# Performance work log

Measured on AMD Instinct MI355X. Metric: run time of the kernel, lower is better.

## Reference

```python
import jax, jax.numpy as jnp
import numpy as np

BN_EPS = 1e-5


def _gcn(x, A, W, gamma, beta):
    # x: [B,N,Cin], A: [B,N,N] -> [B,N,Cout]; BatchNorm1d over (B,N) per channel (train-mode batch stats)
    h = jnp.einsum('bnm,bmc->bnc', A, x @ W)
    mu = h.mean(axis=(0, 1))
    var = h.var(axis=(0, 1))
    h = (h - mu) * jax.lax.rsqrt(var + BN_EPS) * gamma + beta
    return jax.nn.relu(h)  # dropout is identity (drop_prob=0 / eval)


def _ppige(x, A, W0, g0, b0, W_res, g_res, b_res):
    h = _gcn(x, A, W0, g0, b0)
    for i in range(W_res.shape[0]):  # residual GCN stack (num_GCN-1 layers)
        h = _gcn(h, A, W_res[i], g_res[i], b_res[i]) + h
    return h


def _gge(x, w1, b1, w2, b2):
    return jax.nn.relu(jax.nn.relu(x @ w1 + b1) @ w2 + b2)


def _gaga(G, h):
    # G: [B,N,H], h: [B,H]
    att = jax.nn.softmax(jnp.einsum('bnh,bh->bn', G, h), axis=-1)
    return jnp.einsum('bnh,bn->bh', G, att)


def _led(ea, eb, conv_w, conv_b, p1_w, p1_b, p2_w, p2_b):
    # ea, eb: [B, 2H]; Conv1d(2H->2H, k=1) over length-2 axis then MaxPool1d(2)
    stacked = jnp.stack([ea, eb], axis=-1)  # [B, 2H, 2]
    conv = jnp.einsum('oc,bct->bot', conv_w, stacked) + conv_b[None, :, None]
    cnn_x = conv.max(axis=-1)  # [B, 2H]
    x = jax.nn.relu(jnp.concatenate([cnn_x, ea - eb], axis=1) @ p1_w + p1_b)
    return x @ p2_w + p2_b


def setup_inputs() -> dict:
    key = jax.random.key(0)
    ks = jax.random.split(key, 24)
    Bs, N, PPI_in, H, F_in = 8, 2048, 512, 256, 1024
    n_res = 3  # num_GCN - 1
    s = 0.02
    adjA = jax.random.uniform(ks[0], (Bs, N, N), jnp.float32)
    adjB = jax.random.uniform(ks[1], (Bs, N, N), jnp.float32)
    adjA = adjA / adjA.sum(-1, keepdims=True)  # row-normalized for numerical sanity
    adjB = adjB / adjB.sum(-1, keepdims=True)
    return {
        'a': jax.random.normal(ks[2], (Bs, F_in), jnp.float32),
        'bio_a': jax.random.normal(ks[3], (Bs, N, PPI_in), jnp.float32),
        'A': adjA,
        'b': jax.random.normal(ks[4], (Bs, F_in), jnp.float32),
        'bio_b': jax.random.normal(ks[5], (Bs, N, PPI_in), jnp.float32),
        'B': adjB,
        'W0': jax.random.normal(ks[6], (PPI_in, H), jnp.float32) * s,
        'gamma0': jnp.ones((H,), jnp.float32),
        'beta0': jnp.zeros((H,), jnp.float32),
        'W_res': jax.random.normal(ks[7], (n_res, H, H), jnp.float32) * s,
        'gamma_res': jnp.ones((n_res, H), jnp.float32),
        'beta_res': jnp.zeros((n_res, H), jnp.float32),
        'g1_w': jax.random.normal(ks[8], (F_in, 128), jnp.float32) * s,
        'g1_b': jnp.zeros((128,), jnp.float32),
        'g2_w': jax.random.normal(ks[9], (128, H), jnp.float32) * s,
        'g2_b': jnp.zeros((H,), jnp.float32),
        'conv_w': jax.random.normal(ks[10], (2 * H, 2 * H), jnp.float32) * s,
        'conv_b': jnp.zeros((2 * H,), jnp.float32),
        'p1_w': jax.random.normal(ks[11], (4 * H, H), jnp.float32) * s,
        'p1_b': jnp.zeros((H,), jnp.float32),
        'p2_w': jax.random.normal(ks[12], (H, 2), jnp.float32) * s,
        'p2_b': jnp.zeros((2,), jnp.float32),
    }


def reference(a, bio_a, A, b, bio_b, B, W0, gamma0, beta0, W_res, gamma_res, beta_res,
              g1_w, g1_b, g2_w, g2_b, conv_w, conv_b, p1_w, p1_b, p2_w, p2_b):
    Ga = _ppige(bio_a, A, W0, gamma0, beta0, W_res, gamma_res, beta_res)
    Gb = _ppige(bio_b, B, W0, gamma0, beta0, W_res, gamma_res, beta_res)
    ha = _gge(a, g1_w, g1_b, g2_w, g2_b)
    hb = _gge(b, g1_w, g1_b, g2_w, g2_b)
    ea = jnp.concatenate([ha, _gaga(Ga, ha)], axis=-1)
    eb = jnp.concatenate([hb, _gaga(Gb, hb)], axis=-1)
    logits = _led(ea, eb, conv_w, conv_b, p1_w, p1_b, p2_w, p2_b)
    return jax.nn.log_softmax(logits, axis=-1)
```

## Files before the change

kernel.cpp:

```cpp
#include <hip/hip_runtime.h>
#include <hip/hip_bf16.h>
#include <cstdint>

typedef unsigned short u16;
typedef __bf16 bf16x8 __attribute__((ext_vector_type(8)));
typedef float f32x4 __attribute__((ext_vector_type(4)));

typedef __attribute__((address_space(1))) const void* gas_ptr;
typedef __attribute__((address_space(3))) void* las_ptr;

__device__ __forceinline__ u16 f2bf(float f) {
  union { __hip_bfloat16 h; u16 u; } v;
  v.h = __float2bfloat16(f);
  return v.u;
}
__device__ __forceinline__ float bf2f(u16 u) {
  union { unsigned int i; float f; } v;
  v.i = ((unsigned int)u) << 16;
  return v.f;
}

__device__ __forceinline__ void gload16(const u16* g, u16* l) {
  __builtin_amdgcn_global_load_lds((gas_ptr)g, (las_ptr)l, 16, 0, 0);
}

__global__ __launch_bounds__(256) void k_prep_weights(const float* __restrict__ W0,
                                                      const float* __restrict__ Wres,
                                                      u16* __restrict__ W0t,
                                                      u16* __restrict__ Wrt) {
  __shared__ float tile[32][33];
  int y = blockIdx.y;
  const float* src; u16* dst; int R, r0;
  if (y < 16) { src = W0; dst = W0t; R = 512; r0 = y * 32; }
  else {
    int i = (y - 16) >> 3;
    src = Wres + i * 65536; dst = Wrt + i * 65536; R = 256; r0 = ((y - 16) & 7) * 32;
  }
  const int C = 256;
  int c0 = blockIdx.x * 32;
  int tx = threadIdx.x & 31, ty = threadIdx.x >> 5;
#pragma unroll
  for (int i = 0; i < 4; ++i) {
    int r = ty + i * 8;
    tile[r][tx] = src[(long)(r0 + r) * C + c0 + tx];
  }
  __syncthreads();
#pragma unroll
  for (int i = 0; i < 4; ++i) {
    int c = ty + i * 8;
    dst[(long)(c0 + c) * R + r0 + tx] = f2bf(tile[tx][c]);
  }
}

template<int EPI, int SWZ, int CVT>
__global__ __launch_bounds__(256, 3) void k_gemm(
    const u16* __restrict__ A, int lda, long sA,
    const float* __restrict__ Afa, const float* __restrict__ Afb,
    long splitRow, int ldaf, long zrows, u16* __restrict__ AbfOut,
    const u16* __restrict__ Bt, int ldb, long sB,
    u16* __restrict__ C, int ldc, long sC,
    u16* __restrict__ PtOut, int ldpt,
    float* __restrict__ stats, int K) {
  __shared__ __align__(16) u16 smem[24576];
  __shared__ float cs[256];
  const int tid = threadIdx.x;
  const int lane = tid & 63;
  const int wid = tid >> 6;
  const int wm = wid >> 1, wn = wid & 1;

  int bx = blockIdx.x, by = blockIdx.y, bz = blockIdx.z;
  if (SWZ == 1) {
    int lin = bx + 16 * by + 32 * bz;
    int swz = (lin & 7) * 64 + (lin >> 3);
    bx = swz & 15; by = (swz >> 4) & 1; bz = swz >> 5;
  } else if (SWZ == 2) {
    int t = bx; bx = by; by = t;
  }
  const long m0 = (long)bx * 128, n0 = (long)by * 128;
  const int z = bz;
  const u16* Ab = A + (long)z * sA;
  const u16* Btb = Bt + (long)z * sB;

  const int rsub = lane >> 3;
  const int swzcol = ((lane & 7) ^ rsub) * 8;
  const long a_row = m0 + wid * 32 + rsub;
  const long b_row = n0 + wid * 32 + rsub;

  if (EPI == 0) cs[tid] = 0.f;

  const f32x4 zero = {0.f, 0.f, 0.f, 0.f};
  f32x4 acc[4][4];
#pragma unroll
  for (int i = 0; i < 4; ++i)
#pragma unroll
    for (int j = 0; j < 4; ++j) acc[i][j] = zero;

  const int fr = lane & 15;
  const int kgrp = lane >> 4;
  const int swz_rd = lane & 7;
  const int nk = K >> 6;

  float4 rgf[8];
  uint4 rgu[4];

  auto stageB = [&](int bufofs, int k0) {
#pragma unroll
    for (int i = 0; i < 4; ++i)
      gload16(Btb + (b_row + i * 8) * (long)ldb + (k0 + swzcol),
              &smem[bufofs + (wid * 32 + i * 8) * 64]);
  };
  auto loadA = [&](int k0) {
    if constexpr (CVT) {
#pragma unroll
      for (int i = 0; i < 4; ++i) {
        long R = (long)z * zrows + a_row + i * 8;
        const float* sp = (R < splitRow ? Afa + R * (long)ldaf
                                        : Afb + (R - splitRow) * (long)ldaf) + k0 + swzcol;
        rgf[i * 2] = *reinterpret_cast<const float4*>(sp);
        rgf[i * 2 + 1] = *reinterpret_cast<const float4*>(sp + 4);
      }
    } else {
#pragma unroll
      for (int i = 0; i < 4; ++i)
        rgu[i] = *reinterpret_cast<const uint4*>(Ab + (a_row + i * 8) * (long)lda + k0 + swzcol);
    }
  };
  auto writeA = [&](int k0) {
#pragma unroll
    for (int i = 0; i < 4; ++i) {
      uint4 q;
      if constexpr (CVT) {
        union { u16 u[8]; uint4 qq; } o;
        o.u[0] = f2bf(rgf[i*2].x);   o.u[1] = f2bf(rgf[i*2].y);
        o.u[2] = f2bf(rgf[i*2].z);   o.u[3] = f2bf(rgf[i*2].w);
        o.u[4] = f2bf(rgf[i*2+1].x); o.u[5] = f2bf(rgf[i*2+1].y);
        o.u[6] = f2bf(rgf[i*2+1].z); o.u[7] = f2bf(rgf[i*2+1].w);
        q = o.qq;
        if (AbfOut && by == 0) {
          long R = (long)z * zrows + a_row + i * 8;
          *reinterpret_cast<uint4*>(AbfOut + R * (long)ldaf + k0 + swzcol) = q;
        }
      } else {
        q = rgu[i];
      }
      *reinterpret_cast<uint4*>(&smem[(wid * 32 + i * 8) * 64 + lane * 8]) = q;
    }
  };
  auto compute = [&](const u16* Asb, const u16* Bsb) {
#pragma unroll
    for (int ks = 0; ks < 2; ++ks) {
      bf16x8 af[4], bfv[4];
#pragma unroll
      for (int f = 0; f < 4; ++f) {
        int cA = (ks * 4 + kgrp) ^ swz_rd;
        af[f]  = *reinterpret_cast<const bf16x8*>(&Asb[(wm * 64 + f * 16 + fr) * 64 + cA * 8]);
        bfv[f] = *reinterpret_cast<const bf16x8*>(&Bsb[(wn * 64 + f * 16 + fr) * 64 + cA * 8]);
      }
#pragma unroll
      for (int mf = 0; mf < 4; ++mf)
#pragma unroll
        for (int nf = 0; nf < 4; ++nf)
          acc[mf][nf] = __builtin_amdgcn_mfma_f32_16x16x32_bf16(af[mf], bfv[nf], acc[mf][nf], 0, 0, 0);
    }
  };

  stageB(8192, 0);
  loadA(0);
  writeA(0);
  __syncthreads();
  for (int t = 0; t < nk; ++t) {
    const u16* Bsb = &smem[8192 + ((t & 1) << 13)];
    if (t + 1 < nk) {
      stageB(8192 + ((~t & 1) << 13), (t + 1) * 64);
      loadA((t + 1) * 64);
    }
    compute(smem, Bsb);
    __syncthreads();
    if (t + 1 < nk) writeA((t + 1) * 64);
    __syncthreads();
  }

  if (EPI == 0) {
    u16* Cb = C + (long)z * sC;
    const int side = z >> 3;
#pragma unroll
    for (int mf = 0; mf < 4; ++mf) {
      long mrow = m0 + wm * 64 + mf * 16 + kgrp * 4;
#pragma unroll
      for (int nf = 0; nf < 4; ++nf) {
        long ncol = n0 + wn * 64 + nf * 16 + fr;
#pragma unroll
        for (int r = 0; r < 4; ++r)
          Cb[(mrow + r) * ldc + ncol] = f2bf(acc[mf][nf][r]);
      }
    }
#pragma unroll
    for (int nf = 0; nf < 4; ++nf) {
      int cl = wn * 64 + nf * 16 + fr;
      float s = 0.f, q = 0.f;
#pragma unroll
      for (int mf = 0; mf < 4; ++mf)
#pragma unroll
        for (int r = 0; r < 4; ++r) { float v = acc[mf][nf][r]; s += v; q += v * v; }
      atomicAdd(&cs[cl], s);
      atomicAdd(&cs[128 + cl], q);
    }
    __syncthreads();
    if (tid < 128) atomicAdd(&stats[side * 512 + n0 + tid], cs[tid]);
    else           atomicAdd(&stats[side * 512 + 256 + n0 + (tid - 128)], cs[tid]);
  } else {
    u16* Ts = &smem[0];
#pragma unroll
    for (int mf = 0; mf < 4; ++mf)
#pragma unroll
      for (int nf = 0; nf < 4; ++nf) {
        int nl = wn * 64 + nf * 16 + fr;
        int ml = wm * 64 + mf * 16 + kgrp * 4;
#pragma unroll
        for (int r = 0; r < 4; ++r)
          Ts[nl * 136 + ml + r] = f2bf(acc[mf][nf][r]);
      }
    __syncthreads();
    int n = tid >> 1, half = tid & 1;
    const u16* sp = Ts + n * 136 + half * 64;
    u16* dp = PtOut + (long)(n0 + n) * ldpt + m0 + half * 64;
#pragma unroll
    for (int j = 0; j < 8; ++j)
      reinterpret_cast<uint4*>(dp)[j] = reinterpret_cast<const uint4*>(sp)[j];
  }
}

__global__ __launch_bounds__(256) void k_bn_apply(const ushort4* __restrict__ u4,
                                                  ushort4* __restrict__ h4,
                                                  const float* __restrict__ statsL,
                                                  const float* __restrict__ gamma,
                                                  const float* __restrict__ beta, int res) {
  long i = (long)blockIdx.x * 256 + threadIdx.x;
  int side = (int)(i >> 20);
  int c0 = (int)(i & 63) * 4;
  const float* st = statsL + side * 512;
  ushort4 uv = u4[i];
  float vp[4] = { bf2f(uv.x), bf2f(uv.y), bf2f(uv.z), bf2f(uv.w) };
  float rp[4];
#pragma unroll
  for (int j = 0; j < 4; ++j) {
    int c = c0 + j;
    float mu = st[c] * (1.f / 16384.f);
    float var = st[256 + c] * (1.f / 16384.f) - mu * mu;
    float sc = gamma[c] * rsqrtf(var + 1e-5f);
    float sh = beta[c] - mu * sc;
    rp[j] = fmaxf(vp[j] * sc + sh, 0.f);
  }
  if (res) {
    ushort4 hv = h4[i];
    rp[0] += bf2f(hv.x); rp[1] += bf2f(hv.y); rp[2] += bf2f(hv.z); rp[3] += bf2f(hv.w);
  }
  ushort4 o;
  o.x = f2bf(rp[0]); o.y = f2bf(rp[1]); o.z = f2bf(rp[2]); o.w = f2bf(rp[3]);
  h4[i] = o;
}

__global__ __launch_bounds__(256) void k_gge(const float* __restrict__ in_a,
                                             const float* __restrict__ in_b,
                                             const float* __restrict__ w1, const float* __restrict__ b1,
                                             const float* __restrict__ w2, const float* __restrict__ b2,
                                             float* __restrict__ ha) {
  __shared__ float av[1024];
  __shared__ float hid[128];
  int bx = blockIdx.x, t = threadIdx.x;
  const float* ap = ((bx >> 3) ? in_b : in_a) + (bx & 7) * 1024;
  for (int i = t; i < 1024; i += 256) av[i] = ap[i];
  __syncthreads();
  if (t < 128) {
    float s = b1[t];
    for (int c = 0; c < 1024; ++c) s += av[c] * w1[c * 128 + t];
    hid[t] = fmaxf(s, 0.f);
  }
  __syncthreads();
  float s = b2[t];
  for (int c = 0; c < 128; ++c) s += hid[c] * w2[c * 256 + t];
  ha[bx * 256 + t] = fmaxf(s, 0.f);
}

__global__ __launch_bounds__(256) void k_gaga_scores(const u16* __restrict__ h,
                                                     const float* __restrict__ ha,
                                                     float* __restrict__ sc) {
  __shared__ __align__(16) float has[256];
  int bx = blockIdx.x;
  has[threadIdx.x] = ha[bx * 256 + threadIdx.x];
  __syncthreads();
  const u16* G = h + (long)bx * 524288;
  int wv = threadIdx.x >> 6, lane = threadIdx.x & 63;
  float4 h4 = reinterpret_cast<const float4*>(has)[lane];
  for (int i = 0; i < 32; ++i) {
    int n = blockIdx.y * 128 + wv * 32 + i;
    ushort4 v = reinterpret_cast<const ushort4*>(G + (long)n * 256)[lane];
    float d = bf2f(v.x) * h4.x + bf2f(v.y) * h4.y + bf2f(v.z) * h4.z + bf2f(v.w) * h4.w;
#pragma unroll
    for (int o2 = 32; o2 > 0; o2 >>= 1) d += __shfl_down(d, o2);
    if (lane == 0) sc[bx * 2048 + n] = d;
  }
}

__global__ __launch_bounds__(256) void k_softmax2048(const float* __restrict__ sc, float* __restrict__ att) {
  __shared__ float red[256];
  int b = blockIdx.x, t = threadIdx.x;
  const float* s = sc + b * 2048;
  float* o = att + b * 2048;
  float v[8];
  float m = -1e30f;
#pragma unroll
  for (int i = 0; i < 8; ++i) { v[i] = s[t + i * 256]; m = fmaxf(m, v[i]); }
  red[t] = m; __syncthreads();
  for (int o2 = 128; o2 > 0; o2 >>= 1) { if (t < o2) red[t] = fmaxf(red[t], red[t + o2]); __syncthreads(); }
  m = red[0]; __syncthreads();
  float sum = 0.f;
#pragma unroll
  for (int i = 0; i < 8; ++i) { v[i] = expf(v[i] - m); sum += v[i]; }
  red[t] = sum; __syncthreads();
  for (int o2 = 128; o2 > 0; o2 >>= 1) { if (t < o2) red[t] += red[t + o2]; __syncthreads(); }
  float inv = 1.f / red[0];
#pragma unroll
  for (int i = 0; i < 8; ++i) o[t + i * 256] = v[i] * inv;
}

__global__ __launch_bounds__(256) void k_gaga_out(const u16* __restrict__ h,
                                                  const float* __restrict__ att,
                                                  float* __restrict__ ga) {
  __shared__ float atts[128];
  int bx = blockIdx.x, n0 = blockIdx.y * 128, c = threadIdx.x;
  if (threadIdx.x < 128) atts[threadIdx.x] = att[bx * 2048 + n0 + threadIdx.x];
  __syncthreads();
  const u16* base = h + (long)bx * 524288 + (long)n0 * 256 + c;
  float s = 0.f;
#pragma unroll 4
  for (int i = 0; i < 128; ++i) s += bf2f(base[(long)i * 256]) * atts[i];
  atomicAdd(&ga[bx * 256 + c], s);
}

__global__ __launch_bounds__(512) void k_led_conv(const float* __restrict__ ha, const float* __restrict__ ga,
                                                  const float* __restrict__ hb, const float* __restrict__ gb,
                                                  const float* __restrict__ cw, const float* __restrict__ cb,
                                                  float* __restrict__ cnn, float* __restrict__ diff) {
  __shared__ float ea[8][512], eb[8][512];
  int t = threadIdx.x;
  for (int i = t; i < 4096; i += 512) {
    int b = i >> 9, c = i & 511;
    float va = (c < 256) ? ha[b * 256 + c] : ga[b * 256 + c - 256];
    float vb = (c < 256) ? hb[b * 256 + c] : gb[b * 256 + c - 256];
    ea[b][c] = va; eb[b][c] = vb;
    if (blockIdx.x == 0) diff[i] = va - vb;
  }
  __syncthreads();
  int o = blockIdx.x * 64 + (t >> 3), b = t & 7;
  const float* wr = cw + (long)o * 512;
  float s0 = cb[o], s1 = s0;
  for (int c = 0; c < 512; ++c) { float w = wr[c]; s0 += w * ea[b][c]; s1 += w * eb[b][c]; }
  cnn[b * 512 + o] = fmaxf(s0, s1);
}

__global__ __launch_bounds__(256) void k_led_p1(const float* __restrict__ cnn, const float* __restrict__ diff,
                                                const float* __restrict__ w, const float* __restrict__ pb,
                                                float* __restrict__ x) {
  __shared__ float cat[8][1024];
  int t = threadIdx.x;
  for (int i = t; i < 8192; i += 256) {
    int b = i >> 10, c = i & 1023;
    cat[b][c] = (c < 512) ? cnn[b * 512 + c] : diff[b * 512 + c - 512];
  }
  __syncthreads();
  int o = blockIdx.x * 32 + (t >> 3), b = t & 7;
  float s = pb[o];
  for (int c = 0; c < 1024; ++c) s += cat[b][c] * w[c * 256 + o];
  x[b * 256 + o] = fmaxf(s, 0.f);
}

__global__ __launch_bounds__(64) void k_led_final(const float* __restrict__ x,
                                                  const float* __restrict__ p2w, const float* __restrict__ p2b,
                                                  float* __restrict__ out) {
  __shared__ float lg[16];
  int t = threadIdx.x;
  if (t < 16) {
    int b = t >> 1, j = t & 1;
    float s = p2b[j];
    for (int c = 0; c < 256; ++c) s += x[b * 256 + c] * p2w[c * 2 + j];
    lg[t] = s;
  }
  __syncthreads();
  if (t < 8) {
    float l0 = lg[t * 2], l1 = lg[t * 2 + 1];
    float m = fmaxf(l0, l1);
    float lse = m + logf(expf(l0 - m) + expf(l1 - m));
    out[t * 2] = l0 - lse;
    out[t * 2 + 1] = l1 - lse;
  }
}

extern "C" void kernel_launch(void* const* d_in, const int* in_sizes, int n_in,
                              void* d_out, int out_size, void* d_ws, size_t ws_size,
                              hipStream_t stream) {
  const float* in_a   = (const float*)d_in[0];
  const float* bio_a  = (const float*)d_in[1];
  const float* adj_a  = (const float*)d_in[2];
  const float* in_b   = (const float*)d_in[3];
  const float* bio_b  = (const float*)d_in[4];
  const float* adj_b  = (const float*)d_in[5];
  const float* W0     = (const float*)d_in[6];
  const float* gamma0 = (const float*)d_in[7];
  const float* beta0  = (const float*)d_in[8];
  const float* W_res  = (const float*)d_in[9];
  const float* g_res  = (const float*)d_in[10];
  const float* b_res  = (const float*)d_in[11];
  const float* g1_w   = (const float*)d_in[12];
  const float* g1_b   = (const float*)d_in[13];
  const float* g2_w   = (const float*)d_in[14];
  const float* g2_b   = (const float*)d_in[15];
  const float* conv_w = (const float*)d_in[16];
  const float* conv_b = (const float*)d_in[17];
  const float* p1_w   = (const float*)d_in[18];
  const float* p1_b   = (const float*)d_in[19];
  const float* p2_w   = (const float*)d_in[20];
  const float* p2_b   = (const float*)d_in[21];
  float* out = (float*)d_out;

  char* ws = (char*)d_ws;
  size_t off = 0;
  auto alloc = [&](size_t bytes) {
    char* p = ws + off;
    off += (bytes + 255) & ~(size_t)255;
    return p;
  };
  u16*   Abf   = (u16*)  alloc(67108864ull * 2);
  u16*   Pt    = (u16*)  alloc(8388608ull * 2);
  u16*   ubf   = (u16*)  alloc(8388608ull * 2);
  u16*   hbf   = (u16*)  alloc(8388608ull * 2);
  u16*   W0t   = (u16*)  alloc(131072ull * 2);
  u16*   Wrt   = (u16*)  alloc(196608ull * 2);
  float* stats = (float*)alloc(4096 * 4);
  float* gabuf = (float*)alloc(4096 * 4);
  float* hav   = (float*)alloc(4096 * 4);
  float* scb   = (float*)alloc(32768 * 4);
  float* attb  = (float*)alloc(32768 * 4);
  float* cnn   = (float*)alloc(4096 * 4);
  float* diff  = (float*)alloc(4096 * 4);
  float* xbuf  = (float*)alloc(2048 * 4);

  k_prep_weights<<<dim3(8, 40), 256, 0, stream>>>(W0, W_res, W0t, Wrt);
  (void)hipMemsetAsync(stats, 0, 32768, stream);

  for (int layer = 0; layer < 4; ++layer) {
    float* statsL = stats + layer * 1024;
    const float* gm = (layer == 0) ? gamma0 : (g_res + (layer - 1) * 256);
    const float* bt = (layer == 0) ? beta0 : (b_res + (layer - 1) * 256);

    if (layer == 0) {
      k_gemm<1, 2, 1><<<dim3(2, 256, 1), 256, 0, stream>>>(
          nullptr, 0, 0, bio_a, bio_b, 16384L, 512, 0, nullptr,
          W0t, 512, 0, nullptr, 0, 0, Pt, 32768, nullptr, 512);
      k_gemm<0, 1, 1><<<dim3(16, 2, 16), 256, 0, stream>>>(
          nullptr, 0, 0, adj_a, adj_b, 16384L, 2048, 2048, Abf,
          Pt, 32768, 2048, ubf, 256, 524288L, nullptr, 0, statsL, 2048);
    } else {
      const u16* Wt = Wrt + (layer - 1) * 65536;
      k_gemm<1, 2, 0><<<dim3(2, 256, 1), 256, 0, stream>>>(
          hbf, 256, 0, nullptr, nullptr, 0, 0, 0, nullptr,
          Wt, 256, 0, nullptr, 0, 0, Pt, 32768, nullptr, 256);
      k_gemm<0, 1, 0><<<dim3(16, 2, 16), 256, 0, stream>>>(
          Abf, 2048, 4194304L, nullptr, nullptr, 0, 0, 0, nullptr,
          Pt, 32768, 2048, ubf, 256, 524288L, nullptr, 0, statsL, 2048);
    }
    k_bn_apply<<<8192, 256, 0, stream>>>((const ushort4*)ubf, (ushort4*)hbf,
                                         statsL, gm, bt, layer ? 1 : 0);
  }

  k_gge<<<16, 256, 0, stream>>>(in_a, in_b, g1_w, g1_b, g2_w, g2_b, hav);
  k_gaga_scores<<<dim3(16, 16), 256, 0, stream>>>(hbf, hav, scb);
  k_softmax2048<<<16, 256, 0, stream>>>(scb, attb);
  k_gaga_out<<<dim3(16, 16), 256, 0, stream>>>(hbf, attb, gabuf);

  k_led_conv<<<8, 512, 0, stream>>>(hav, gabuf, hav + 2048, gabuf + 2048, conv_w, conv_b, cnn, diff);
  k_led_p1<<<8, 256, 0, stream>>>(cnn, diff, p1_w, p1_b, xbuf);
  k_led_final<<<1, 64, 0, stream>>>(xbuf, p2_w, p2_b, out);
}
```

Measured before the change: 563.9 us.

## Double-buffer A tiles via direct-to-LDS loads with manual waitcnt pipeline

Splits shared memory into four 8K buffers so both A and B tiles are double-buffered. The non-converting path now loads A with global_load_lds straight into LDS instead of going through registers. Both paths use explicit vmcnt waits and a single barrier per stage instead of two __syncthreads. This targets the register round-trip and extra barrier in the main loop, and it also drops the occupancy hint from launch bounds. The trade-offs are higher LDS use (64KB, up from 48KB), which may lower occupancy, and reliance on hand-counted vmcnt values that must match the number of outstanding loads.

```diff
diff --git a/kernel.cpp b/kernel.cpp
--- a/kernel.cpp
+++ b/kernel.cpp
@@ -53,7 +53,7 @@
 }
 
 template<int EPI, int SWZ, int CVT>
-__global__ __launch_bounds__(256, 3) void k_gemm(
+__global__ __launch_bounds__(256) void k_gemm(
     const u16* __restrict__ A, int lda, long sA,
     const float* __restrict__ Afa, const float* __restrict__ Afb,
     long splitRow, int ldaf, long zrows, u16* __restrict__ AbfOut,
@@ -61,7 +61,7 @@
     u16* __restrict__ C, int ldc, long sC,
     u16* __restrict__ PtOut, int ldpt,
     float* __restrict__ stats, int K) {
-  __shared__ __align__(16) u16 smem[24576];
+  __shared__ __align__(16) u16 smem[4][8192];
   __shared__ float cs[256];
   const int tid = threadIdx.x;
   const int lane = tid & 63;
@@ -101,49 +101,42 @@
   const int nk = K >> 6;
 
   float4 rgf[8];
-  uint4 rgu[4];
-
-  auto stageB = [&](int bufofs, int k0) {
+
+  auto stageA = [&](int buf, int k0) {
+#pragma unroll
+    for (int i = 0; i < 4; ++i)
+      gload16(Ab + (a_row + i * 8) * (long)lda + (k0 + swzcol),
+              &smem[buf][(wid * 32 + i * 8) * 64]);
+  };
+  auto stageB = [&](int buf, int k0) {
 #pragma unroll
     for (int i = 0; i < 4; ++i)
       gload16(Btb + (b_row + i * 8) * (long)ldb + (k0 + swzcol),
-              &smem[bufofs + (wid * 32 + i * 8) * 64]);
+              &smem[2 + buf][(wid * 32 + i * 8) * 64]);
   };
   auto loadA = [&](int k0) {
-    if constexpr (CVT) {
-#pragma unroll
-      for (int i = 0; i < 4; ++i) {
+#pragma unroll
+    for (int i = 0; i < 4; ++i) {
+      long R = (long)z * zrows + a_row + i * 8;
+      const float* sp = (R < splitRow ? Afa + R * (long)ldaf
+                                      : Afb + (R - splitRow) * (long)ldaf) + k0 + swzcol;
+      rgf[i * 2] = *reinterpret_cast<const float4*>(sp);
+      rgf[i * 2 + 1] = *reinterpret_cast<const float4*>(sp + 4);
+    }
+  };
+  auto writeA = [&](int buf, int k0) {
+#pragma unroll
+    for (int i = 0; i < 4; ++i) {
+      union { u16 u[8]; uint4 qq; } o;
+      o.u[0] = f2bf(rgf[i*2].x);   o.u[1] = f2bf(rgf[i*2].y);
+      o.u[2] = f2bf(rgf[i*2].z);   o.u[3] = f2bf(rgf[i*2].w);
+      o.u[4] = f2bf(rgf[i*2+1].x); o.u[5] = f2bf(rgf[i*2+1].y);
+      o.u[6] = f2bf(rgf[i*2+1].z); o.u[7] = f2bf(rgf[i*2+1].w);
+      if (AbfOut && by == 0) {
         long R = (long)z * zrows + a_row + i * 8;
-        const float* sp = (R < splitRow ? Afa + R * (long)ldaf
-                                        : Afb + (R - splitRow) * (long)ldaf) + k0 + swzcol;
-        rgf[i * 2] = *reinterpret_cast<const float4*>(sp);
-        rgf[i * 2 + 1] = *reinterpret_cast<const float4*>(sp + 4);
-      }
-    } else {
-#pragma unroll
-      for (int i = 0; i < 4; ++i)
-        rgu[i] = *reinterpret_cast<const uint4*>(Ab + (a_row + i * 8) * (long)lda + k0 + swzcol);
-    }
-  };
-  auto writeA = [&](int k0) {
-#pragma unroll
-    for (int i = 0; i < 4; ++i) {
-      uint4 q;
-      if constexpr (CVT) {
-        union { u16 u[8]; uint4 qq; } o;
-        o.u[0] = f2bf(rgf[i*2].x);   o.u[1] = f2bf(rgf[i*2].y);
-        o.u[2] = f2bf(rgf[i*2].z);   o.u[3] = f2bf(rgf[i*2].w);
-        o.u[4] = f2bf(rgf[i*2+1].x); o.u[5] = f2bf(rgf[i*2+1].y);
-        o.u[6] = f2bf(rgf[i*2+1].z); o.u[7] = f2bf(rgf[i*2+1].w);
-        q = o.qq;
-        if (AbfOut && by == 0) {
-          long R = (long)z * zrows + a_row + i * 8;
-          *reinterpret_cast<uint4*>(AbfOut + R * (long)ldaf + k0 + swzcol) = q;
-        }
-      } else {
-        q = rgu[i];
-      }
-      *reinterpret_cast<uint4*>(&smem[(wid * 32 + i * 8) * 64 + lane * 8]) = q;
+        *reinterpret_cast<uint4*>(AbfOut + R * (long)ldaf + k0 + swzcol) = o.qq;
+      }
+      *reinterpret_cast<uint4*>(&smem[buf][(wid * 32 + i * 8) * 64 + lane * 8]) = o.qq;
     }
   };
   auto compute = [&](const u16* Asb, const u16* Bsb) {
@@ -164,20 +157,41 @@
     }
   };
 
-  stageB(8192, 0);
-  loadA(0);
-  writeA(0);
-  __syncthreads();
-  for (int t = 0; t < nk; ++t) {
-    const u16* Bsb = &smem[8192 + ((t & 1) << 13)];
-    if (t + 1 < nk) {
-      stageB(8192 + ((~t & 1) << 13), (t + 1) * 64);
-      loadA((t + 1) * 64);
-    }
-    compute(smem, Bsb);
-    __syncthreads();
-    if (t + 1 < nk) writeA((t + 1) * 64);
-    __syncthreads();
+  if constexpr (CVT) {
+    loadA(0); stageB(0, 0); writeA(0, 0);
+    for (int t = 0; t < nk; ++t) {
+      int cur = t & 1, nxt = cur ^ 1;
+      if (t + 1 < nk) {
+        loadA((t + 1) * 64);
+        stageB(nxt, (t + 1) * 64);
+        asm volatile("s_waitcnt vmcnt(12) lgkmcnt(0)" ::: "memory");
+      } else {
+        asm volatile("s_waitcnt vmcnt(0) lgkmcnt(0)" ::: "memory");
+      }
+      __builtin_amdgcn_s_barrier();
+      __builtin_amdgcn_sched_barrier(0);
+      compute(smem[cur], smem[2 + cur]);
+      if (t + 1 < nk) writeA(nxt, (t + 1) * 64);
+      asm volatile("s_waitcnt lgkmcnt(0)" ::: "memory");
+      __builtin_amdgcn_s_barrier();
+    }
+  } else {
+    stageA(0, 0); stageB(0, 0);
+    for (int t = 0; t < nk; ++t) {
+      int cur = t & 1, nxt = cur ^ 1;
+      if (t + 1 < nk) {
+        stageA(nxt, (t + 1) * 64);
+        stageB(nxt, (t + 1) * 64);
+        asm volatile("s_waitcnt vmcnt(8) lgkmcnt(0)" ::: "memory");
+      } else {
+        asm volatile("s_waitcnt vmcnt(0) lgkmcnt(0)" ::: "memory");
+      }
+      __builtin_amdgcn_s_barrier();
+      __builtin_amdgcn_sched_barrier(0);
+      compute(smem[cur], smem[2 + cur]);
+      asm volatile("s_waitcnt lgkmcnt(0)" ::: "memory");
+      __builtin_amdgcn_s_barrier();
+    }
   }
 
   if (EPI == 0) {
@@ -209,7 +223,7 @@
     if (tid < 128) atomicAdd(&stats[side * 512 + n0 + tid], cs[tid]);
     else           atomicAdd(&stats[side * 512 + 256 + n0 + (tid - 128)], cs[tid]);
   } else {
-    u16* Ts = &smem[0];
+    u16* Ts = &smem[0][0];
 #pragma unroll
     for (int mf = 0; mf < 4; ++mf)
 #pragma unroll
```

New measurement: 551.3 us. -2.2%, faster.

## Single-buffer GEMM LDS with direct-to-LDS A loads to raise occupancy

Applied to the files above, without the earlier changes.

Removes the double-buffered B tile so LDS per block shrinks, and raises the launch-bounds occupancy hint from 3 to 4 blocks per CU. In the non-convert path, A is now staged straight into LDS with global_load_lds instead of passing through registers. The price is the lost software pipelining: each iteration loads, syncs, computes and syncs again, so global latency is no longer hidden inside a block and must be covered by the extra resident blocks.

```diff
diff --git a/kernel.cpp b/kernel.cpp
--- a/kernel.cpp
+++ b/kernel.cpp
@@ -53,7 +53,7 @@
 }
 
 template<int EPI, int SWZ, int CVT>
-__global__ __launch_bounds__(256, 3) void k_gemm(
+__global__ __launch_bounds__(256, 4) void k_gemm(
     const u16* __restrict__ A, int lda, long sA,
     const float* __restrict__ Afa, const float* __restrict__ Afb,
     long splitRow, int ldaf, long zrows, u16* __restrict__ AbfOut,
@@ -61,7 +61,7 @@
     u16* __restrict__ C, int ldc, long sC,
     u16* __restrict__ PtOut, int ldpt,
     float* __restrict__ stats, int K) {
-  __shared__ __align__(16) u16 smem[24576];
+  __shared__ __align__(16) u16 smem[17408];
   __shared__ float cs[256];
   const int tid = threadIdx.x;
   const int lane = tid & 63;
@@ -101,52 +101,47 @@
   const int nk = K >> 6;
 
   float4 rgf[8];
-  uint4 rgu[4];
-
-  auto stageB = [&](int bufofs, int k0) {
+
+  auto stageA = [&](int k0) {
+#pragma unroll
+    for (int i = 0; i < 4; ++i)
+      gload16(Ab + (a_row + i * 8) * (long)lda + (k0 + swzcol),
+              &smem[(wid * 32 + i * 8) * 64]);
+  };
+  auto stageB = [&](int k0) {
 #pragma unroll
     for (int i = 0; i < 4; ++i)
       gload16(Btb + (b_row + i * 8) * (long)ldb + (k0 + swzcol),
-              &smem[bufofs + (wid * 32 + i * 8) * 64]);
+              &smem[8192 + (wid * 32 + i * 8) * 64]);
   };
   auto loadA = [&](int k0) {
-    if constexpr (CVT) {
-#pragma unroll
-      for (int i = 0; i < 4; ++i) {
+#pragma unroll
+    for (int i = 0; i < 4; ++i) {
+      long R = (long)z * zrows + a_row + i * 8;
+      const float* sp = (R < splitRow ? Afa + R * (long)ldaf
+                                      : Afb + (R - splitRow) * (long)ldaf) + k0 + swzcol;
+      rgf[i * 2] = *reinterpret_cast<const float4*>(sp);
+      rgf[i * 2 + 1] = *reinterpret_cast<const float4*>(sp + 4);
+    }
+  };
+  auto writeA = [&](int k0) {
+#pragma unroll
+    for (int i = 0; i < 4; ++i) {
+      union { u16 u[8]; uint4 qq; } o;
+      o.u[0] = f2bf(rgf[i*2].x);   o.u[1] = f2bf(rgf[i*2].y);
+      o.u[2] = f2bf(rgf[i*2].z);   o.u[3] = f2bf(rgf[i*2].w);
+      o.u[4] = f2bf(rgf[i*2+1].x); o.u[5] = f2bf(rgf[i*2+1].y);
+      o.u[6] = f2bf(rgf[i*2+1].z); o.u[7] = f2bf(rgf[i*2+1].w);
+      if (AbfOut && by == 0) {
         long R = (long)z * zrows + a_row + i * 8;
-        const float* sp = (R < splitRow ? Afa + R * (long)ldaf
-                                        : Afb + (R - splitRow) * (long)ldaf) + k0 + swzcol;
-        rgf[i * 2] = *reinterpret_cast<const float4*>(sp);
-        rgf[i * 2 + 1] = *reinterpret_cast<const float4*>(sp + 4);
+        *reinterpret_cast<uint4*>(AbfOut + R * (long)ldaf + k0 + swzcol) = o.qq;
       }
-    } else {
-#pragma unroll
-      for (int i = 0; i < 4; ++i)
-        rgu[i] = *reinterpret_cast<const uint4*>(Ab + (a_row + i * 8) * (long)lda + k0 + swzcol);
-    }
-  };
-  auto writeA = [&](int k0) {
-#pragma unroll
-    for (int i = 0; i < 4; ++i) {
-      uint4 q;
-      if constexpr (CVT) {
-        union { u16 u[8]; uint4 qq; } o;
-        o.u[0] = f2bf(rgf[i*2].x);   o.u[1] = f2bf(rgf[i*2].y);
-        o.u[2] = f2bf(rgf[i*2].z);   o.u[3] = f2bf(rgf[i*2].w);
-        o.u[4] = f2bf(rgf[i*2+1].x); o.u[5] = f2bf(rgf[i*2+1].y);
-        o.u[6] = f2bf(rgf[i*2+1].z); o.u[7] = f2bf(rgf[i*2+1].w);
-        q = o.qq;
-        if (AbfOut && by == 0) {
-          long R = (long)z * zrows + a_row + i * 8;
-          *reinterpret_cast<uint4*>(AbfOut + R * (long)ldaf + k0 + swzcol) = q;
-        }
-      } else {
-        q = rgu[i];
-      }
-      *reinterpret_cast<uint4*>(&smem[(wid * 32 + i * 8) * 64 + lane * 8]) = q;
-    }
-  };
-  auto compute = [&](const u16* Asb, const u16* Bsb) {
+      *reinterpret_cast<uint4*>(&smem[(wid * 32 + i * 8) * 64 + lane * 8]) = o.qq;
+    }
+  };
+  auto compute = [&]() {
+    const u16* Asb = &smem[0];
+    const u16* Bsb = &smem[8192];
 #pragma unroll
     for (int ks = 0; ks < 2; ++ks) {
       bf16x8 af[4], bfv[4];
@@ -164,19 +159,17 @@
     }
   };
 
-  stageB(8192, 0);
-  loadA(0);
-  writeA(0);
-  __syncthreads();
   for (int t = 0; t < nk; ++t) {
-    const u16* Bsb = &smem[8192 + ((t & 1) << 13)];
-    if (t + 1 < nk) {
-      stageB(8192 + ((~t & 1) << 13), (t + 1) * 64);
-      loadA((t + 1) * 64);
-    }
-    compute(smem, Bsb);
+    if constexpr (CVT) {
+      loadA(t * 64);
+      stageB(t * 64);
+      writeA(t * 64);
+    } else {
+      stageA(t * 64);
+      stageB(t * 64);
+    }
     __syncthreads();
-    if (t + 1 < nk) writeA((t + 1) * 64);
+    compute();
     __syncthreads();
   }
 
```

New measurement: 598.3 us. 6.1% more time.
